# Kernel tuning notes

Measured on AMD Instinct MI355X. Metric: run time of the kernel, lower is better.

The kernel has to match this reference:

```python
import jax, jax.numpy as jnp
import numpy as np

B, L, K, G, C, S = 1024, 32, 8, 8, 128, 32
D_IN = 2 * L + K + S  # masked z (L) + mask (L) + target (K) + shared (S)
TAU = 1.0
EPS = 1e-5
NEG_INF = -1e9  # stands in for torch's -9e15 diagonal fill; sigmoid(-1e9)=0


def setup_inputs() -> dict:
    key = jax.random.key(0)
    ks = jax.random.split(key, 24)
    eye = jnp.eye(K, dtype=bool)
    kaiming = lambda k, shape: jax.random.uniform(k, shape, jnp.float32, -1.0, 1.0) * np.sqrt(6.0 / shape[-1])
    return {
        "z_sample": jax.random.normal(ks[0], (B, L), jnp.float32),
        "target": jax.random.randint(ks[1], (B,), 0, K),
        "z_mean": jax.random.normal(ks[2], (B, L), jnp.float32),
        "z_logstd": 0.1 * jax.random.normal(ks[3], (B, L), jnp.float32),
        "z_shared": jax.random.normal(ks[4], (B, S), jnp.float32),
        "u_gumbel": jax.random.uniform(ks[5], (B, L, K), jnp.float32),
        "u_adj": jax.random.uniform(ks[6], (B, G, K, K), jnp.float32),
        "target_params": 0.1 * jax.random.normal(ks[7], (L, K), jnp.float32),
        "enco_theta": jnp.where(eye, NEG_INF, jax.random.normal(ks[8], (K, K), jnp.float32)),
        "enco_gamma": jnp.where(eye, NEG_INF, jax.random.normal(ks[9], (K, K), jnp.float32)),
        "W1": kaiming(ks[10], (L, C, D_IN)),
        "b1": jnp.zeros((L, C), jnp.float32),
        "gn1_w": jnp.ones((L, C), jnp.float32),
        "gn1_b": jnp.zeros((L, C), jnp.float32),
        "W2": kaiming(ks[11], (L, C, C)),
        "b2": jnp.zeros((L, C), jnp.float32),
        "gn2_w": jnp.ones((L, C), jnp.float32),
        "gn2_b": jnp.zeros((L, C), jnp.float32),
        "W3": 0.01 * jax.random.normal(ks[12], (L, 2, C), jnp.float32),
        "b3": jnp.zeros((L, 2), jnp.float32),
        "tanh_scale": jnp.zeros((L, 2), jnp.float32),
    }


def _mv_linear(x, W, b):
    # x: [B,G,L,d_in], W: [L,d_out,d_in] -> [B,G,L,d_out]  (per-latent independent linear)
    return jnp.einsum("bgld,lhd->bglh", x, W) + b


def _mv_groupnorm(x, w, b):
    # GroupNorm(L groups over L*C channels) == per-(sample, latent) normalization over C
    mu = x.mean(-1, keepdims=True)
    var = ((x - mu) ** 2).mean(-1, keepdims=True)
    return (x - mu) * jax.lax.rsqrt(var + EPS) * w + b


def reference(z_sample, target, z_mean, z_logstd, z_shared, u_gumbel, u_adj,
              target_params, enco_theta, enco_gamma,
              W1, b1, gn1_w, gn1_b, W2, b2, gn2_w, gn2_b, W3, b3, tanh_scale):
    dt = z_sample.dtype
    target_oh = jax.nn.one_hot(target, K, dtype=dt)  # [B,K]

    # hard gumbel-softmax with straight-through estimator: psi assigns latents to causal vars
    g = -jnp.log(-jnp.log(u_gumbel + 1e-10) + 1e-10)
    soft = jax.nn.softmax((target_params[None] + g) / TAU, axis=-1)  # [B,L,K]
    hard = jax.nn.one_hot(jnp.argmax(soft, axis=-1), K, dtype=dt)
    psi = hard + soft - jax.lax.stop_gradient(soft)  # [B,L,K]

    # ENCO graph sampling: edge prob = sigmoid(theta)*sigmoid(gamma), Bernoulli samples
    edge_prob = jax.nn.sigmoid(enco_theta) * jax.nn.sigmoid(enco_gamma)  # [K,K]
    adj = (u_adj < edge_prob[None, None]).astype(dt)  # [B,G,K,K], adj[k,l]=1: k->l

    # latent-level parent mask: mask[b,g,i,j]=1 iff latent j is a parent of latent i
    latent_mask = jnp.einsum("bil,bgkl,bjk->bgij", psi, adj, psi)  # [B,G,L,L]
    latent_mask = latent_mask * (1.0 - jnp.eye(L, dtype=dt))

    # per-latent network input: [masked parents, mask, intervention indicator, shared]
    z_masked = latent_mask * z_sample[:, None, None, :]                        # [B,G,L,L]
    t_inp = jnp.broadcast_to((psi * target_oh[:, None, :])[:, None], (B, G, L, K))
    zs = jnp.broadcast_to(z_shared[:, None, None, :], (B, G, L, S))
    s_inp = jnp.concatenate([z_masked, latent_mask, t_inp, zs], axis=-1)       # [B,G,L,D_IN]

    h = jax.nn.silu(_mv_groupnorm(_mv_linear(s_inp, W1, b1), gn1_w, gn1_b))
    h = jax.nn.silu(_mv_groupnorm(_mv_linear(h, W2, b2), gn2_w, gn2_b))
    h = _mv_linear(h, W3, b3)                                                  # [B,G,L,2]
    sc = jnp.exp(tanh_scale)                                                   # [L,2]
    h = jnp.tanh(h / sc) * sc                                                  # MultivarStableTanh
    prior_mean, prior_logstd = h[..., 0], h[..., 1]                            # [B,G,L]

    # KL(q(z) || p(z)) per latent, averaged over graph samples, summed over latents
    var_q = jnp.exp(2.0 * z_logstd)[:, None]                                   # [B,1,L]
    kld = (prior_logstd - z_logstd[:, None]
           + (var_q + (z_mean[:, None] - prior_mean) ** 2) / (2.0 * jnp.exp(2.0 * prior_logstd))
           - 0.5)                                                              # [B,G,L]
    return kld.mean(axis=1).sum(axis=-1)                                       # [B]
```

## Files before the change

### kernel.cpp

```cpp
#include <hip/hip_runtime.h>
#include <hip/hip_bf16.h>

#define B_DIM 1024
#define L_DIM 32
#define K_DIM 8
#define G_DIM 8
#define C_DIM 128
#define S_DIM 32
#define DIN   104

typedef __bf16  bf16x8 __attribute__((ext_vector_type(8)));
typedef float   f32x4  __attribute__((ext_vector_type(4)));

union frag_u { uint4 u; bf16x8 v; };

static __device__ __forceinline__ unsigned int pk2(float a, float b) {
    __hip_bfloat162 h = __float22bfloat162_rn(make_float2(a, b));
    union { __hip_bfloat162 h; unsigned int u; } v; v.h = h; return v.u;
}
static __device__ __forceinline__ bf16x8 ld_frag(const unsigned short* p) {
    frag_u t; t.u = *(const uint4*)p; return t.v;
}
static __device__ __forceinline__ bf16x8 u2f(uint4 u) {
    frag_u t; t.u = u; return t.v;
}
static __device__ __forceinline__ float siluf(float x) {
    return __fdividef(x, 1.0f + __expf(-x));
}

__global__ __launch_bounds__(256) void prep_kernel(
    const float* __restrict__ u_gumbel,
    const float* __restrict__ u_adj,
    const float* __restrict__ target_params,
    const float* __restrict__ enco_theta,
    const float* __restrict__ enco_gamma,
    const int*   __restrict__ target,
    const float* __restrict__ W1,
    const float* __restrict__ W2,
    float*       __restrict__ out,
    unsigned char* __restrict__ cvarpk,
    unsigned int*  __restrict__ wsmask,
    unsigned short* __restrict__ wscr)
{
    const int t = threadIdx.x;
    if (blockIdx.x >= 1024) {
        int gtid  = (blockIdx.x - 1024) * 256 + t;
        int lane  = gtid & 63;
        int ks    = (gtid >> 6) & 3;
        int mt    = (gtid >> 8) & 3;
        int wm    = (gtid >> 10) & 1;
        int l     = (gtid >> 11) & 31;
        int which = gtid >> 16;
        int m  = 16 * (4 * wm + mt) + (lane & 15);
        int k0 = ks * 32 + (lane >> 4) * 8;
        uint4 o;
        if (which == 0) {
            if (k0 >= 104) {
                o = make_uint4(0u, 0u, 0u, 0u);
            } else {
                const float* p = W1 + (size_t)l * 13312 + m * 104 + k0;
                float4 a = *(const float4*)p, bq = *(const float4*)(p + 4);
                o = make_uint4(pk2(a.x, a.y), pk2(a.z, a.w), pk2(bq.x, bq.y), pk2(bq.z, bq.w));
            }
        } else {
            const float* p = W2 + (size_t)l * 16384 + m * 128 + k0;
            float4 a = *(const float4*)p, bq = *(const float4*)(p + 4);
            o = make_uint4(pk2(a.x, a.y), pk2(a.z, a.w), pk2(bq.x, bq.y), pk2(bq.z, bq.w));
        }
        *(uint4*)(wscr + (size_t)gtid * 8) = o;
        return;
    }

    __shared__ double ep[64];
    __shared__ unsigned char cv8[32];
    __shared__ unsigned long long adjb[8];
    const int b = blockIdx.x;
    if (t < 64) {
        double th = (double)enco_theta[t];
        double ga = (double)enco_gamma[t];
        ep[t] = (1.0 / (1.0 + exp(-th))) * (1.0 / (1.0 + exp(-ga)));
    }
    if (t == 0) out[b] = 0.0f;
    __syncthreads();

    {
        const int l = t >> 3, k = t & 7;
        double u = (double)u_gumbel[b * 256 + t];
        double g = -log(-log(u + 1e-10) + 1e-10);
        double v = (double)target_params[t] + g;
        int bk = k;
        #pragma unroll
        for (int off = 1; off < 8; off <<= 1) {
            double ov = __shfl_xor(v, off, 64);
            int   obk = __shfl_xor(bk, off, 64);
            if (ov > v || (ov == v && obk < bk)) { v = ov; bk = obk; }
        }
        if (k == 0) {
            int tg = target[b];
            unsigned char pkd = (unsigned char)(bk | ((bk == tg) ? 8 : 0));
            cvarpk[b * 32 + l] = pkd;
            cv8[l] = pkd;
        }
    }
    {
        const int wv = t >> 6, lane = t & 63;
        #pragma unroll
        for (int q = 0; q < 2; ++q) {
            int gg = wv + 4 * q;
            double u = (double)u_adj[b * 512 + gg * 64 + lane];
            unsigned long long m = __ballot(u < ep[lane]);
            if (lane == 0) adjb[gg] = m;
        }
    }
    __syncthreads();

    {
        const int g = t >> 5, l = t & 31;
        int lam = cv8[l] & 7;
        unsigned long long bits = adjb[g] >> lam;
        unsigned int mask = 0u;
        #pragma unroll
        for (int j = 0; j < 32; ++j) {
            int kap = cv8[j] & 7;
            mask |= ((unsigned int)(bits >> (kap * 8)) & 1u) << j;
        }
        mask &= ~(1u << l);
        wsmask[l * 8192 + b * 8 + g] = mask;
    }
}

__global__ __launch_bounds__(256, 2) void fused_kernel(
    const float* __restrict__ z_sample,
    const float* __restrict__ z_mean,
    const float* __restrict__ z_logstd,
    const float* __restrict__ z_shared,
    const float* __restrict__ pb1,
    const float* __restrict__ g1w,
    const float* __restrict__ g1b,
    const float* __restrict__ pb2,
    const float* __restrict__ g2w,
    const float* __restrict__ g2b,
    const float* __restrict__ W3,
    const float* __restrict__ pb3,
    const float* __restrict__ tsc,
    const unsigned short* __restrict__ wscr,
    const unsigned char*  __restrict__ cvarpk,
    const unsigned int*   __restrict__ wsmask,
    float* __restrict__ out)
{
    __shared__ __align__(16) unsigned short XH[4][32][136];
    __shared__ float p_g1w[128], p_g1b[128], p_b1[128];
    __shared__ float p_g2w[128], p_g2b[128], p_b2[128];
    __shared__ float p_w3[2][128];
    __shared__ float p_b3[2], p_ts[2];
    __shared__ unsigned int  msk[128];
    __shared__ unsigned char cvl[16];

    const int tid  = threadIdx.x;
    const int w    = tid >> 6, lane = tid & 63;
    const int lo   = lane & 15, hi = lane >> 4;
    const int l    = blockIdx.x & 31;
    const int grp  = blockIdx.x >> 5;

    if (tid < 128) {
        int c = tid;
        p_g1w[c] = g1w[l * 128 + c];  p_g1b[c] = g1b[l * 128 + c];
        p_b1[c]  = pb1[l * 128 + c];  p_w3[0][c] = W3[l * 256 + c];
        msk[c]   = wsmask[l * 8192 + grp * 128 + c];
    } else {
        int c = tid - 128;
        p_g2w[c] = g2w[l * 128 + c];  p_g2b[c] = g2b[l * 128 + c];
        p_b2[c]  = pb2[l * 128 + c];  p_w3[1][c] = W3[l * 256 + 128 + c];
    }
    if (tid < 16) cvl[tid] = cvarpk[(size_t)(grp * 16 + tid) * 32 + l];
    if (tid == 0) {
        p_b3[0] = pb3[l * 2];  p_b3[1] = pb3[l * 2 + 1];
        p_ts[0] = tsc[l * 2];  p_ts[1] = tsc[l * 2 + 1];
    }
    __syncthreads();

    bf16x8 bq[2][4];
    #pragma unroll
    for (int nt = 0; nt < 2; ++nt) {
        int r  = w * 32 + nt * 16 + lo;
        int bl = r >> 3;
        int bg = grp * 16 + bl;
        unsigned int m32 = msk[r];
        unsigned int mq  = (m32 >> (hi * 8)) & 0xffu;
        const float4* zp = (const float4*)(z_sample + bg * 32 + hi * 8);
        float4 za = zp[0], zb = zp[1];
        uint4 f0;
        f0.x = pk2((mq & 1u)   ? za.x : 0.f, (mq & 2u)   ? za.y : 0.f);
        f0.y = pk2((mq & 4u)   ? za.z : 0.f, (mq & 8u)   ? za.w : 0.f);
        f0.z = pk2((mq & 16u)  ? zb.x : 0.f, (mq & 32u)  ? zb.y : 0.f);
        f0.w = pk2((mq & 64u)  ? zb.z : 0.f, (mq & 128u) ? zb.w : 0.f);
        uint4 f1;
        f1.x = ((mq & 1u)   ? 0x3F80u : 0u) | ((mq & 2u)   ? 0x3F800000u : 0u);
        f1.y = ((mq & 4u)   ? 0x3F80u : 0u) | ((mq & 8u)   ? 0x3F800000u : 0u);
        f1.z = ((mq & 16u)  ? 0x3F80u : 0u) | ((mq & 32u)  ? 0x3F800000u : 0u);
        f1.w = ((mq & 64u)  ? 0x3F80u : 0u) | ((mq & 128u) ? 0x3F800000u : 0u);
        unsigned int cb8 = cvl[bl];
        int lam = cb8 & 7, tf = (cb8 >> 3) & 1;
        int zsb = (hi == 0) ? 24 : (hi - 1) * 8;
        const float4* sp = (const float4*)(z_shared + bg * 32 + zsb);
        float4 sa = sp[0], sb = sp[1];
        uint4 fz;
        fz.x = pk2(sa.x, sa.y); fz.y = pk2(sa.z, sa.w);
        fz.z = pk2(sb.x, sb.y); fz.w = pk2(sb.z, sb.w);
        unsigned int ohw = tf ? (0x3F80u << ((lam & 1) << 4)) : 0u;
        int lq = lam >> 1;
        uint4 fo;
        fo.x = (lq == 0) ? ohw : 0u;
        fo.y = (lq == 1) ? ohw : 0u;
        fo.z = (lq == 2) ? ohw : 0u;
        fo.w = (lq == 3) ? ohw : 0u;
        bool h0 = (hi == 0);
        uint4 f2, f3;
        f2.x = h0 ? fo.x : fz.x;  f2.y = h0 ? fo.y : fz.y;
        f2.z = h0 ? fo.z : fz.z;  f2.w = h0 ? fo.w : fz.w;
        f3.x = h0 ? fz.x : 0u;    f3.y = h0 ? fz.y : 0u;
        f3.z = h0 ? fz.z : 0u;    f3.w = h0 ? fz.w : 0u;
        bq[nt][0] = u2f(f0); bq[nt][1] = u2f(f1);
        bq[nt][2] = u2f(f2); bq[nt][3] = u2f(f3);
    }

    const float inv128 = 1.0f / 128.0f;

    f32x4 acc[8][2];
    #pragma unroll
    for (int cb = 0; cb < 8; ++cb)
        #pragma unroll
        for (int nt = 0; nt < 2; ++nt) acc[cb][nt] = (f32x4){0.f, 0.f, 0.f, 0.f};
    {
        const unsigned short* w1p = wscr + (size_t)(l * 32) * 512 + lane * 8;
        #pragma unroll
        for (int ks = 0; ks < 4; ++ks) {
            bf16x8 wf[8];
            #pragma unroll
            for (int cb = 0; cb < 8; ++cb) wf[cb] = ld_frag(w1p + (cb * 4 + ks) * 512);
            #pragma unroll
            for (int cb = 0; cb < 8; ++cb)
                #pragma unroll
                for (int nt = 0; nt < 2; ++nt)
                    acc[cb][nt] = __builtin_amdgcn_mfma_f32_16x16x32_bf16(
                        wf[cb], bq[nt][ks], acc[cb][nt], 0, 0, 0);
        }
    }

    float s1[2] = {0.f, 0.f}, s2[2] = {0.f, 0.f};
    #pragma unroll
    for (int cb = 0; cb < 8; ++cb) {
        float4 b4 = *(const float4*)&p_b1[cb * 16 + hi * 4];
        #pragma unroll
        for (int rg = 0; rg < 4; ++rg) {
            float bias = ((const float*)&b4)[rg];
            #pragma unroll
            for (int nt = 0; nt < 2; ++nt) {
                float v = acc[cb][nt][rg] + bias;
                acc[cb][nt][rg] = v;
                s1[nt] += v;  s2[nt] += v * v;
            }
        }
    }
    float mu[2], rstd[2];
    #pragma unroll
    for (int nt = 0; nt < 2; ++nt) {
        s1[nt] += __shfl_xor(s1[nt], 16, 64);  s1[nt] += __shfl_xor(s1[nt], 32, 64);
        s2[nt] += __shfl_xor(s2[nt], 16, 64);  s2[nt] += __shfl_xor(s2[nt], 32, 64);
        float m_  = s1[nt] * inv128;
        float var = s2[nt] * inv128 - m_ * m_;
        mu[nt] = m_;  rstd[nt] = rsqrtf(var + 1e-5f);
    }
    #pragma unroll
    for (int cb = 0; cb < 8; ++cb) {
        float4 gw4 = *(const float4*)&p_g1w[cb * 16 + hi * 4];
        float4 gb4 = *(const float4*)&p_g1b[cb * 16 + hi * 4];
        #pragma unroll
        for (int nt = 0; nt < 2; ++nt) {
            float sl[4];
            #pragma unroll
            for (int rg = 0; rg < 4; ++rg) {
                float x = (acc[cb][nt][rg] - mu[nt]) * rstd[nt] * ((const float*)&gw4)[rg]
                          + ((const float*)&gb4)[rg];
                sl[rg] = siluf(x);
            }
            *(uint2*)&XH[w][nt * 16 + lo][cb * 16 + hi * 4] =
                make_uint2(pk2(sl[0], sl[1]), pk2(sl[2], sl[3]));
        }
    }

    #pragma unroll
    for (int cb = 0; cb < 8; ++cb)
        #pragma unroll
        for (int nt = 0; nt < 2; ++nt) acc[cb][nt] = (f32x4){0.f, 0.f, 0.f, 0.f};
    {
        const unsigned short* w2p = wscr + (size_t)((32 + l) * 32) * 512 + lane * 8;
        #pragma unroll
        for (int ks = 0; ks < 4; ++ks) {
            bf16x8 wf[8];
            #pragma unroll
            for (int cb = 0; cb < 8; ++cb) wf[cb] = ld_frag(w2p + (cb * 4 + ks) * 512);
            bf16x8 bf0 = ld_frag(&XH[w][lo][ks * 32 + hi * 8]);
            bf16x8 bf1 = ld_frag(&XH[w][16 + lo][ks * 32 + hi * 8]);
            #pragma unroll
            for (int cb = 0; cb < 8; ++cb) {
                acc[cb][0] = __builtin_amdgcn_mfma_f32_16x16x32_bf16(
                    wf[cb], bf0, acc[cb][0], 0, 0, 0);
                acc[cb][1] = __builtin_amdgcn_mfma_f32_16x16x32_bf16(
                    wf[cb], bf1, acc[cb][1], 0, 0, 0);
            }
        }
    }

    float t1[2] = {0.f, 0.f}, t2[2] = {0.f, 0.f};
    #pragma unroll
    for (int cb = 0; cb < 8; ++cb) {
        float4 b4 = *(const float4*)&p_b2[cb * 16 + hi * 4];
        #pragma unroll
        for (int rg = 0; rg < 4; ++rg) {
            float bias = ((const float*)&b4)[rg];
            #pragma unroll
            for (int nt = 0; nt < 2; ++nt) {
                float v = acc[cb][nt][rg] + bias;
                acc[cb][nt][rg] = v;
                t1[nt] += v;  t2[nt] += v * v;
            }
        }
    }
    float mu2[2], rstd2[2];
    #pragma unroll
    for (int nt = 0; nt < 2; ++nt) {
        t1[nt] += __shfl_xor(t1[nt], 16, 64);  t1[nt] += __shfl_xor(t1[nt], 32, 64);
        t2[nt] += __shfl_xor(t2[nt], 16, 64);  t2[nt] += __shfl_xor(t2[nt], 32, 64);
        float m_  = t1[nt] * inv128;
        float var = t2[nt] * inv128 - m_ * m_;
        mu2[nt] = m_;  rstd2[nt] = rsqrtf(var + 1e-5f);
    }
    float pmp[2] = {0.f, 0.f}, plp[2] = {0.f, 0.f};
    #pragma unroll
    for (int cb = 0; cb < 8; ++cb) {
        float4 gw4 = *(const float4*)&p_g2w[cb * 16 + hi * 4];
        float4 gb4 = *(const float4*)&p_g2b[cb * 16 + hi * 4];
        float4 w04 = *(const float4*)&p_w3[0][cb * 16 + hi * 4];
        float4 w14 = *(const float4*)&p_w3[1][cb * 16 + hi * 4];
        #pragma unroll
        for (int rg = 0; rg < 4; ++rg) {
            float wg = ((const float*)&gw4)[rg], gb = ((const float*)&gb4)[rg];
            float w0 = ((const float*)&w04)[rg], w1 = ((const float*)&w14)[rg];
            #pragma unroll
            for (int nt = 0; nt < 2; ++nt) {
                float x  = (acc[cb][nt][rg] - mu2[nt]) * rstd2[nt] * wg + gb;
                float sl = siluf(x);
                pmp[nt] += sl * w0;
                plp[nt] += sl * w1;
            }
        }
    }
    #pragma unroll
    for (int nt = 0; nt < 2; ++nt) {
        pmp[nt] += __shfl_xor(pmp[nt], 16, 64);  pmp[nt] += __shfl_xor(pmp[nt], 32, 64);
        plp[nt] += __shfl_xor(plp[nt], 16, 64);  plp[nt] += __shfl_xor(plp[nt], 32, 64);
    }

    {
        float sc0 = __expf(p_ts[0]), sc1 = __expf(p_ts[1]);
        float is0 = __expf(-p_ts[0]), is1 = __expf(-p_ts[1]);
        #pragma unroll
        for (int nt = 0; nt < 2; ++nt) {
            float pm = pmp[nt] + p_b3[0];
            float pl = plp[nt] + p_b3[1];
            float e0 = __expf(2.0f * pm * is0);
            pm = (1.0f - 2.0f * __fdividef(1.0f, e0 + 1.0f)) * sc0;
            float e1 = __expf(2.0f * pl * is1);
            pl = (1.0f - 2.0f * __fdividef(1.0f, e1 + 1.0f)) * sc1;
            int r  = w * 32 + nt * 16 + lo;
            int bg = grp * 16 + (r >> 3);
            float zm = z_mean[bg * 32 + l];
            float zl = z_logstd[bg * 32 + l];
            float vq = __expf(2.0f * zl);
            float d  = zm - pm;
            float kld = pl - zl + (vq + d * d) * 0.5f * __expf(-2.0f * pl) - 0.5f;
            kld += __shfl_xor(kld, 1, 64);
            kld += __shfl_xor(kld, 2, 64);
            kld += __shfl_xor(kld, 4, 64);
            if (hi == 0 && (lo & 7) == 0) atomicAdd(&out[bg], kld * 0.125f);
        }
    }
}

extern "C" void kernel_launch(void* const* d_in, const int* in_sizes, int n_in,
                              void* d_out, int out_size, void* d_ws, size_t ws_size,
                              hipStream_t stream) {
    const float* z_sample      = (const float*)d_in[0];
    const int*   target        = (const int*)d_in[1];
    const float* z_mean        = (const float*)d_in[2];
    const float* z_logstd      = (const float*)d_in[3];
    const float* z_shared      = (const float*)d_in[4];
    const float* u_gumbel      = (const float*)d_in[5];
    const float* u_adj         = (const float*)d_in[6];
    const float* target_params = (const float*)d_in[7];
    const float* enco_theta    = (const float*)d_in[8];
    const float* enco_gamma    = (const float*)d_in[9];
    const float* W1            = (const float*)d_in[10];
    const float* pb1           = (const float*)d_in[11];
    const float* g1w           = (const float*)d_in[12];
    const float* g1b           = (const float*)d_in[13];
    const float* W2            = (const float*)d_in[14];
    const float* pb2           = (const float*)d_in[15];
    const float* g2w           = (const float*)d_in[16];
    const float* g2b           = (const float*)d_in[17];
    const float* W3            = (const float*)d_in[18];
    const float* pb3           = (const float*)d_in[19];
    const float* tsc           = (const float*)d_in[20];

    unsigned char* cvarpk = (unsigned char*)d_ws;
    unsigned int*  wsmask = (unsigned int*)((char*)d_ws + 32768);
    unsigned short* wscr  = (unsigned short*)((char*)d_ws + 32768 + 1048576);

    prep_kernel<<<1536, 256, 0, stream>>>(u_gumbel, u_adj, target_params,
                                          enco_theta, enco_gamma, target,
                                          W1, W2, (float*)d_out,
                                          cvarpk, wsmask, wscr);
    fused_kernel<<<2048, 256, 0, stream>>>(z_sample, z_mean, z_logstd, z_shared,
                                           pb1, g1w, g1b, pb2, g2w, g2b,
                                           W3, pb3, tsc, wscr, cvarpk, wsmask,
                                           (float*)d_out);
}
```

Baseline: 175.1 us.

## Use fast float Gumbel argmax with double fallback, raise occupancy, split weight loads

The Gumbel argmax in the prep kernel now uses float fast-log instead of double log, and falls back to the double path only when the top two candidates are within a small margin. The fused kernel's launch bounds move from 2 to 3 blocks per SIMD, and the weight fragment loads in both MFMA loops are split into halves of 4 to cut register pressure. The fallback keeps argmax selection exact in practice, but near-ties beyond the threshold could still differ. Higher occupancy may also cause register spilling.

```diff
diff --git a/kernel.cpp b/kernel.cpp
--- a/kernel.cpp
+++ b/kernel.cpp
@@ -85,15 +85,31 @@
 
     {
         const int l = t >> 3, k = t & 7;
-        double u = (double)u_gumbel[b * 256 + t];
-        double g = -log(-log(u + 1e-10) + 1e-10);
-        double v = (double)target_params[t] + g;
-        int bk = k;
+        float uf = u_gumbel[b * 256 + t];
+        float gf = -__logf(-__logf(uf + 1e-10f) + 1e-10f);
+        float vf = target_params[t] + gf;
+        float vm = vf; int bk = k;
         #pragma unroll
         for (int off = 1; off < 8; off <<= 1) {
-            double ov = __shfl_xor(v, off, 64);
-            int   obk = __shfl_xor(bk, off, 64);
-            if (ov > v || (ov == v && obk < bk)) { v = ov; bk = obk; }
+            float ov = __shfl_xor(vm, off, 64);
+            int  obk = __shfl_xor(bk, off, 64);
+            if (ov > vm || (ov == vm && obk < bk)) { vm = ov; bk = obk; }
+        }
+        int amb = ((k != bk) && (vm - vf < 1e-3f)) ? 1 : 0;
+        #pragma unroll
+        for (int off = 1; off < 8; off <<= 1) amb |= __shfl_xor(amb, off, 64);
+        if (amb) {
+            double ud = (double)uf;
+            double gd = -log(-log(ud + 1e-10) + 1e-10);
+            double vd = (double)target_params[t] + gd;
+            int bk2 = k;
+            #pragma unroll
+            for (int off = 1; off < 8; off <<= 1) {
+                double ov = __shfl_xor(vd, off, 64);
+                int   obk = __shfl_xor(bk2, off, 64);
+                if (ov > vd || (ov == vd && obk < bk2)) { vd = ov; bk2 = obk; }
+            }
+            bk = bk2;
         }
         if (k == 0) {
             int tg = target[b];
@@ -129,7 +145,7 @@
     }
 }
 
-__global__ __launch_bounds__(256, 2) void fused_kernel(
+__global__ __launch_bounds__(256, 3) void fused_kernel(
     const float* __restrict__ z_sample,
     const float* __restrict__ z_mean,
     const float* __restrict__ z_logstd,
@@ -235,15 +251,21 @@
         const unsigned short* w1p = wscr + (size_t)(l * 32) * 512 + lane * 8;
         #pragma unroll
         for (int ks = 0; ks < 4; ++ks) {
-            bf16x8 wf[8];
-            #pragma unroll
-            for (int cb = 0; cb < 8; ++cb) wf[cb] = ld_frag(w1p + (cb * 4 + ks) * 512);
-            #pragma unroll
-            for (int cb = 0; cb < 8; ++cb)
+            #pragma unroll
+            for (int half = 0; half < 2; ++half) {
+                bf16x8 wf[4];
                 #pragma unroll
-                for (int nt = 0; nt < 2; ++nt)
-                    acc[cb][nt] = __builtin_amdgcn_mfma_f32_16x16x32_bf16(
-                        wf[cb], bq[nt][ks], acc[cb][nt], 0, 0, 0);
+                for (int q = 0; q < 4; ++q)
+                    wf[q] = ld_frag(w1p + ((half * 4 + q) * 4 + ks) * 512);
+                #pragma unroll
+                for (int q = 0; q < 4; ++q) {
+                    int cb = half * 4 + q;
+                    acc[cb][0] = __builtin_amdgcn_mfma_f32_16x16x32_bf16(
+                        wf[q], bq[0][ks], acc[cb][0], 0, 0, 0);
+                    acc[cb][1] = __builtin_amdgcn_mfma_f32_16x16x32_bf16(
+                        wf[q], bq[1][ks], acc[cb][1], 0, 0, 0);
+                }
+            }
         }
     }
 
@@ -297,17 +319,22 @@
         const unsigned short* w2p = wscr + (size_t)((32 + l) * 32) * 512 + lane * 8;
         #pragma unroll
         for (int ks = 0; ks < 4; ++ks) {
-            bf16x8 wf[8];
-            #pragma unroll
-            for (int cb = 0; cb < 8; ++cb) wf[cb] = ld_frag(w2p + (cb * 4 + ks) * 512);
             bf16x8 bf0 = ld_frag(&XH[w][lo][ks * 32 + hi * 8]);
             bf16x8 bf1 = ld_frag(&XH[w][16 + lo][ks * 32 + hi * 8]);
             #pragma unroll
-            for (int cb = 0; cb < 8; ++cb) {
-                acc[cb][0] = __builtin_amdgcn_mfma_f32_16x16x32_bf16(
-                    wf[cb], bf0, acc[cb][0], 0, 0, 0);
-                acc[cb][1] = __builtin_amdgcn_mfma_f32_16x16x32_bf16(
-                    wf[cb], bf1, acc[cb][1], 0, 0, 0);
+            for (int half = 0; half < 2; ++half) {
+                bf16x8 wf[4];
+                #pragma unroll
+                for (int q = 0; q < 4; ++q)
+                    wf[q] = ld_frag(w2p + ((half * 4 + q) * 4 + ks) * 512);
+                #pragma unroll
+                for (int q = 0; q < 4; ++q) {
+                    int cb = half * 4 + q;
+                    acc[cb][0] = __builtin_amdgcn_mfma_f32_16x16x32_bf16(
+                        wf[q], bf0, acc[cb][0], 0, 0, 0);
+                    acc[cb][1] = __builtin_amdgcn_mfma_f32_16x16x32_bf16(
+                        wf[q], bf1, acc[cb][1], 0, 0, 0);
+                }
             }
         }
     }
```

Result: faster. 169.8 us (-3.0%).
